# Optimization experiments

Measured on AMD Instinct MI355X. Metric: run time of the kernel, lower is better.

The kernel has to match this reference:

```python
import jax, jax.numpy as jnp
import numpy as np

HID = 2048; NH = 16; NKV = 2; HD = 128; G = NH // NKV
SEC = (16, 24, 24)  # sums to 64 = HD/2
EPS = 1e-6
B, S = 2, 1024


def _reorder(table):
    # table: [3, B, S, HD]; interleave sections picking axis i%3 per chunk
    chunks = []
    idx = 0
    for _ in range(2):
        for sec in SEC:
            chunks.append(table[..., idx:idx + sec])
            idx += sec
    return jnp.concatenate([c[i % len(SEC)] for i, c in enumerate(chunks)], axis=-1)  # [B,S,HD]


def rotate_half(x):
    x1, x2 = jnp.split(x, 2, axis=-1)
    return jnp.concatenate((-x2, x1), axis=-1)


def rms_norm(x, gamma):
    var = jnp.mean(jnp.square(x), axis=-1, keepdims=True)
    return gamma * (x * jax.lax.rsqrt(var + EPS))


def setup_inputs() -> dict:
    key = jax.random.key(0)
    ks = jax.random.split(key, 12)
    x = jax.random.normal(ks[0], (B, S, HID), dtype=jnp.float32)
    ang = jax.random.uniform(ks[1], (3, B, S, HD), dtype=jnp.float32) * 6.28318
    cos = jnp.cos(ang)
    sin = jnp.sin(ang)
    mask = jnp.ones((B, S), dtype=jnp.float32)
    sc = 0.02
    q_w = jax.random.normal(ks[2], (HID, NH * HD), dtype=jnp.float32) * sc
    q_b = jnp.zeros((NH * HD,), dtype=jnp.float32)
    k_w = jax.random.normal(ks[3], (HID, NKV * HD), dtype=jnp.float32) * sc
    k_b = jnp.zeros((NKV * HD,), dtype=jnp.float32)
    v_w = jax.random.normal(ks[4], (HID, NKV * HD), dtype=jnp.float32) * sc
    v_b = jnp.zeros((NKV * HD,), dtype=jnp.float32)
    q_gamma = jnp.ones((HD,), dtype=jnp.float32)
    k_gamma = jnp.ones((HD,), dtype=jnp.float32)
    o_w = jax.random.normal(ks[5], (NH * HD, HID), dtype=jnp.float32) * sc
    return {"x": x, "cos": cos, "sin": sin, "mask": mask,
            "q_w": q_w, "q_b": q_b, "k_w": k_w, "k_b": k_b,
            "v_w": v_w, "v_b": v_b, "q_gamma": q_gamma, "k_gamma": k_gamma,
            "o_w": o_w}


def reference(x, cos, sin, mask, q_w, q_b, k_w, k_b, v_w, v_b, q_gamma, k_gamma, o_w):
    b, s, _ = x.shape
    # QKV projections
    q = (x @ q_w + q_b).reshape(b, s, NH, HD)
    k = (x @ k_w + k_b).reshape(b, s, NKV, HD)
    v = (x @ v_w + v_b).reshape(b, s, NKV, HD)
    # per-head RMSNorm on q, k
    q = rms_norm(q, q_gamma)
    k = rms_norm(k, k_gamma)
    q = jnp.transpose(q, (0, 2, 1, 3))  # [B,NH,S,HD]
    k = jnp.transpose(k, (0, 2, 1, 3))  # [B,NKV,S,HD]
    v = jnp.transpose(v, (0, 2, 1, 3))
    # multimodal RoPE
    cos_f = _reorder(cos)[:, None, :, :]  # [B,1,S,HD]
    sin_f = _reorder(sin)[:, None, :, :]
    q = q * cos_f + rotate_half(q) * sin_f
    k = k * cos_f + rotate_half(k) * sin_f
    # key-mask zeroing and effective lengths
    eff = mask.sum(axis=-1).astype(jnp.int32)  # [B]
    bm = mask[:, None, :, None]
    k = k * bm
    v = v * bm
    hist = (jnp.arange(s)[None, :] < eff[:, None]).astype(jnp.float32)  # [B,S]
    # GQA attention scores in fp32
    qg = q.reshape(b, NKV, G, s, HD)
    scores = jnp.einsum('bngqd,bnkd->bngqk', qg, k,
                        precision=jax.lax.Precision.HIGHEST) * (HD ** -0.5)
    scores = scores.reshape(b, NH, s, s)
    scores = scores + (1.0 - hist)[:, None, None, :] * -1e9
    causal = jnp.tril(jnp.ones((s, s), dtype=jnp.float32))
    scores = scores + (1.0 - causal)[None, None, :, :] * -1e9
    aw = jax.nn.softmax(scores, axis=-1)
    # weighted values
    out = jnp.einsum('bngqk,bnkd->bngqd', aw.reshape(b, NKV, G, s, s), v,
                     precision=jax.lax.Precision.HIGHEST)
    out = out.reshape(b, NH, s, HD)
    out = jnp.transpose(out, (0, 2, 1, 3)).reshape(b, s, NH * HD)
    return out @ o_w
```

## Files before the change

kernel.cpp:

```cpp
#include <hip/hip_runtime.h>

typedef __attribute__((ext_vector_type(8))) short bf16x8;
typedef __attribute__((ext_vector_type(4))) float f32x4;

#define MFMA16(a, b, c) __builtin_amdgcn_mfma_f32_16x16x32_bf16(a, b, c, 0, 0, 0)

__device__ inline short f2bf(float f) {
  union { float f; unsigned u; } v;
  v.f = f;
  unsigned r = v.u + 0x7FFF + ((v.u >> 16) & 1);
  return (short)(r >> 16);
}
__device__ inline float bf2f(short s) {
  union { unsigned u; float f; } v;
  v.u = ((unsigned)(unsigned short)s) << 16;
  return v.f;
}
#define GLD_LDS16(g, l)                                                        \
  __builtin_amdgcn_global_load_lds(                                            \
      (const __attribute__((address_space(1))) unsigned int*)(g),              \
      (__attribute__((address_space(3))) unsigned int*)(l), 16, 0, 0)

__device__ __forceinline__ void raw_barrier() {
  __asm__ volatile("" ::: "memory");
  __builtin_amdgcn_s_barrier();
  __asm__ volatile("" ::: "memory");
}

__global__ __launch_bounds__(256) void prep_kernel(
    const float* __restrict__ x, const float* __restrict__ q_w,
    const float* __restrict__ k_w, const float* __restrict__ v_w,
    const float* __restrict__ o_w, const float* __restrict__ q_b,
    const float* __restrict__ k_b, const float* __restrict__ v_b,
    short* __restrict__ xb, short* __restrict__ wqkv_t, short* __restrict__ wo_t,
    float* __restrict__ biasAll) {
  __shared__ float t[64][65];
  int bid = blockIdx.x;
  if (bid == 6400) {
    for (int i = threadIdx.x; i < 2560; i += 256) {
      float v = (i < 2048) ? q_b[i] : (i < 2304 ? k_b[i - 2048] : v_b[i - 2304]);
      biasAll[i] = v;
    }
    return;
  }
  if (bid < 4096) {
    int i = (bid * 256 + threadIdx.x) * 4;
    float4 f = *(const float4*)&x[i];
    short4 o;
    o.x = f2bf(f.x); o.y = f2bf(f.y); o.z = f2bf(f.z); o.w = f2bf(f.w);
    *(short4*)&xb[i] = o;
    return;
  }
  bid -= 4096;
  const float* src;
  short* dst;
  int C, bx, by;
  if (bid < 1024) {
    src = q_w; dst = wqkv_t; C = 2048;
    bx = (bid & 31) * 64; by = (bid >> 5) * 64;
  } else if (bid < 1152) {
    bid -= 1024;
    src = k_w; dst = wqkv_t + (size_t)2048 * 2048; C = 256;
    bx = (bid & 3) * 64; by = (bid >> 2) * 64;
  } else if (bid < 1280) {
    bid -= 1152;
    src = v_w; dst = wqkv_t + (size_t)2304 * 2048; C = 256;
    bx = (bid & 3) * 64; by = (bid >> 2) * 64;
  } else {
    bid -= 1280;
    src = o_w; dst = wo_t; C = 2048;
    bx = (bid & 31) * 64; by = (bid >> 5) * 64;
  }
  const int R = 2048;
  const int tx = threadIdx.x & 15;
  const int ty = threadIdx.x >> 4;
#pragma unroll
  for (int i = 0; i < 4; i++) {
    int row = ty + i * 16;
    float4 f = *(const float4*)&src[(size_t)(by + row) * C + bx + tx * 4];
    t[row][tx * 4 + 0] = f.x;
    t[row][tx * 4 + 1] = f.y;
    t[row][tx * 4 + 2] = f.z;
    t[row][tx * 4 + 3] = f.w;
  }
  __syncthreads();
#pragma unroll
  for (int i = 0; i < 4; i++) {
    int c = ty + i * 16;
    short4 o;
    o.x = f2bf(t[tx * 4 + 0][c]);
    o.y = f2bf(t[tx * 4 + 1][c]);
    o.z = f2bf(t[tx * 4 + 2][c]);
    o.w = f2bf(t[tx * 4 + 3][c]);
    *(short4*)&dst[(size_t)(bx + c) * R + by + tx * 4] = o;
  }
}

__global__ __launch_bounds__(256) void gemm_qkv_kernel(const short* __restrict__ A,
                                                       const short* __restrict__ B,
                                                       short* __restrict__ Cs,
                                                       const float* __restrict__ bias,
                                                       int N, int gx, int gy, int P) {
  __shared__ __align__(16) short As[4][64 * 32];
  __shared__ __align__(16) short Bs[4][128 * 32];
  const int bid = blockIdx.x;
  const int xcd = bid & 7, idx = bid >> 3;
  const int colsPerX = gx >> 1, rowsPerX = gy >> 2;
  const int xt = (xcd & 1) * colsPerX + idx % colsPerX;
  const int yt = (xcd >> 1) * rowsPerX + idx / colsPerX;
  const int tid = threadIdx.x;
  const int lane = tid & 63, wave = tid >> 6;
  const int quad = lane >> 4, l16 = lane & 15;
  const int m0 = yt * 64, n0 = xt * 128;
  const int wm = (wave >> 1) * 32, wn = (wave & 1) * 64;
  const int r0 = tid >> 2, c0 = (tid & 3) * 8;
  const int ca = ((tid & 3) ^ ((r0 >> 1) & 3)) * 8;
  const size_t arow = (size_t)(m0 + r0) * 2048;
  const size_t brow0 = (size_t)(n0 + r0) * 2048, brow1 = (size_t)(n0 + r0 + 64) * 2048;
  f32x4 acc[2][4];
#pragma unroll
  for (int mi = 0; mi < 2; mi++)
#pragma unroll
    for (int ni = 0; ni < 4; ni++) acc[mi][ni] = (f32x4){0.f, 0.f, 0.f, 0.f};

#pragma unroll
  for (int st = 0; st < 4; st++) {
    const int kk = st * 32 + ca;
    GLD_LDS16(&A[arow + kk], &As[st][r0 * 32 + c0]);
    GLD_LDS16(&B[brow0 + kk], &Bs[st][r0 * 32 + c0]);
    GLD_LDS16(&B[brow1 + kk], &Bs[st][(r0 + 64) * 32 + c0]);
  }

  const int sx = (l16 >> 1) & 3;
  for (int p = 0; p < P; p++) {
    if (p < P - 1) {
      __asm__ volatile("s_waitcnt vmcnt(6)" ::: "memory");
    } else {
      __asm__ volatile("s_waitcnt vmcnt(0)" ::: "memory");
    }
    raw_barrier();
#pragma unroll
    for (int j = 0; j < 2; j++) {
      const int cur = (2 * p + j) & 3;
      bf16x8 af[2], bfr[4];
#pragma unroll
      for (int mi = 0; mi < 2; mi++)
        af[mi] = *(const bf16x8*)&As[cur][(wm + mi * 16 + l16) * 32 + ((quad ^ sx) * 8)];
#pragma unroll
      for (int ni = 0; ni < 4; ni++)
        bfr[ni] = *(const bf16x8*)&Bs[cur][(wn + ni * 16 + l16) * 32 + ((quad ^ sx) * 8)];
#pragma unroll
      for (int mi = 0; mi < 2; mi++)
#pragma unroll
        for (int ni = 0; ni < 4; ni++)
          acc[mi][ni] = MFMA16(af[mi], bfr[ni], acc[mi][ni]);
    }
    __asm__ volatile("s_waitcnt lgkmcnt(0)" ::: "memory");
    raw_barrier();
    if (p < P - 2) {
#pragma unroll
      for (int j = 0; j < 2; j++) {
        const int st = 2 * p + 4 + j;
        const int slot = st & 3;
        const int kk = st * 32 + ca;
        GLD_LDS16(&A[arow + kk], &As[slot][r0 * 32 + c0]);
        GLD_LDS16(&B[brow0 + kk], &Bs[slot][r0 * 32 + c0]);
        GLD_LDS16(&B[brow1 + kk], &Bs[slot][(r0 + 64) * 32 + c0]);
      }
    }
  }
#pragma unroll
  for (int mi = 0; mi < 2; mi++)
#pragma unroll
    for (int ni = 0; ni < 4; ni++) {
      const int col = n0 + wn + ni * 16 + l16;
      const float bv = bias[col];
#pragma unroll
      for (int r = 0; r < 4; r++)
        Cs[(size_t)(m0 + wm + mi * 16 + quad * 4 + r) * N + col] =
            f2bf(acc[mi][ni][r] + bv);
    }
}

__global__ __launch_bounds__(256) void gemm_db_kernel(const short* __restrict__ A,
                                                      const short* __restrict__ B,
                                                      float* __restrict__ C, int N,
                                                      int gx, int gy, int P) {
  __shared__ __align__(16) short As[4][64 * 32];
  __shared__ __align__(16) short Bs[4][128 * 32];
  const int bid = blockIdx.x;
  const int xcd = bid & 7, idx = bid >> 3;
  const int colsPerX = gx >> 1, rowsPerX = gy >> 2;
  const int xt = (xcd & 1) * colsPerX + idx % colsPerX;
  const int yt = (xcd >> 1) * rowsPerX + idx / colsPerX;
  const int tid = threadIdx.x;
  const int lane = tid & 63, wave = tid >> 6;
  const int quad = lane >> 4, l16 = lane & 15;
  const int m0 = yt * 64, n0 = xt * 128;
  const int wm = (wave >> 1) * 32, wn = (wave & 1) * 64;
  const int r0 = tid >> 2, c0 = (tid & 3) * 8;
  const int ca = ((tid & 3) ^ ((r0 >> 1) & 3)) * 8;
  const size_t arow = (size_t)(m0 + r0) * 2048;
  const size_t brow0 = (size_t)(n0 + r0) * 2048, brow1 = (size_t)(n0 + r0 + 64) * 2048;
  f32x4 acc[2][4];
#pragma unroll
  for (int mi = 0; mi < 2; mi++)
#pragma unroll
    for (int ni = 0; ni < 4; ni++) acc[mi][ni] = (f32x4){0.f, 0.f, 0.f, 0.f};

#pragma unroll
  for (int st = 0; st < 4; st++) {
    const int kk = st * 32 + ca;
    GLD_LDS16(&A[arow + kk], &As[st][r0 * 32 + c0]);
    GLD_LDS16(&B[brow0 + kk], &Bs[st][r0 * 32 + c0]);
    GLD_LDS16(&B[brow1 + kk], &Bs[st][(r0 + 64) * 32 + c0]);
  }

  const int sx = (l16 >> 1) & 3;
  for (int p = 0; p < P; p++) {
    if (p < P - 1) {
      __asm__ volatile("s_waitcnt vmcnt(6)" ::: "memory");
    } else {
      __asm__ volatile("s_waitcnt vmcnt(0)" ::: "memory");
    }
    raw_barrier();
#pragma unroll
    for (int j = 0; j < 2; j++) {
      const int cur = (2 * p + j) & 3;
      bf16x8 af[2], bfr[4];
#pragma unroll
      for (int mi = 0; mi < 2; mi++)
        af[mi] = *(const bf16x8*)&As[cur][(wm + mi * 16 + l16) * 32 + ((quad ^ sx) * 8)];
#pragma unroll
      for (int ni = 0; ni < 4; ni++)
        bfr[ni] = *(const bf16x8*)&Bs[cur][(wn + ni * 16 + l16) * 32 + ((quad ^ sx) * 8)];
#pragma unroll
      for (int mi = 0; mi < 2; mi++)
#pragma unroll
        for (int ni = 0; ni < 4; ni++)
          acc[mi][ni] = MFMA16(af[mi], bfr[ni], acc[mi][ni]);
    }
    __asm__ volatile("s_waitcnt lgkmcnt(0)" ::: "memory");
    raw_barrier();
    if (p < P - 2) {
#pragma unroll
      for (int j = 0; j < 2; j++) {
        const int st = 2 * p + 4 + j;
        const int slot = st & 3;
        const int kk = st * 32 + ca;
        GLD_LDS16(&A[arow + kk], &As[slot][r0 * 32 + c0]);
        GLD_LDS16(&B[brow0 + kk], &Bs[slot][r0 * 32 + c0]);
        GLD_LDS16(&B[brow1 + kk], &Bs[slot][(r0 + 64) * 32 + c0]);
      }
    }
  }
#pragma unroll
  for (int mi = 0; mi < 2; mi++)
#pragma unroll
    for (int ni = 0; ni < 4; ni++)
#pragma unroll
      for (int r = 0; r < 4; r++)
        C[(size_t)(m0 + wm + mi * 16 + quad * 4 + r) * N + n0 + wn + ni * 16 + l16] =
            acc[mi][ni][r];
}

__global__ __launch_bounds__(256) void postv_kv_kernel(
    const short* __restrict__ qkvb, const float* __restrict__ kg,
    const float* __restrict__ cosb, const float* __restrict__ sinb,
    const float* __restrict__ maskp, short* __restrict__ ko, short* __restrict__ vtb) {
  __shared__ short t[32][33];
  const int bid = blockIdx.x;
  if (bid < 1024) {
    const int rid = bid * 4 + (threadIdx.x >> 6);
    const int lane = threadIdx.x & 63;
    const int slot = rid >> 11;
    const int bs = rid & 2047;
    const int b = bs >> 10, s = bs & 1023;
    const short* row = qkvb + (size_t)bs * 2560 + 2048 + slot * 128;
    float v0 = bf2f(row[lane]);
    float v1 = bf2f(row[64 + lane]);
    float ss = v0 * v0 + v1 * v1;
#pragma unroll
    for (int o = 1; o < 64; o <<= 1) ss += __shfl_xor(ss, o);
    float r = rsqrtf(ss * (1.0f / 128.0f) + 1e-6f);
    v0 = kg[lane] * v0 * r;
    v1 = kg[64 + lane] * v1 * r;
    int sel = (lane < 16) ? 0 : (lane < 40) ? 1 : 2;
    size_t ci = ((size_t)(sel * 2 + b) * 1024 + s) * 128 + lane;
    float c0 = cosb[ci], s0 = sinb[ci], c1 = cosb[ci + 64], s1 = sinb[ci + 64];
    const float mk = maskp[bs];
    float o0 = (v0 * c0 - v1 * s0) * mk;
    float o1 = (v1 * c1 + v0 * s1) * mk;
    short* dst = ko + (((size_t)(b * 2 + slot) * 1024) + s) * 128;
    dst[lane] = f2bf(o0);
    dst[64 + lane] = f2bf(o1);
    return;
  }
  const int b2 = bid - 1024;
  const int d0 = (b2 & 3) * 32;
  const int s0 = ((b2 >> 2) & 31) * 32;
  const int bz = b2 >> 7;
  const int bq = bz >> 1, kv = bz & 1;
  const int tx = threadIdx.x & 31;
  const int ty = threadIdx.x >> 5;
#pragma unroll
  for (int i = 0; i < 4; i++) {
    int s = s0 + ty + i * 8;
    size_t qi = ((size_t)(bq * 1024 + s)) * 2560 + 2304 + kv * 128 + d0 + tx;
    float val = bf2f(qkvb[qi]);
    t[ty + i * 8][tx] = f2bf(val * maskp[bq * 1024 + s]);
  }
  __syncthreads();
#pragma unroll
  for (int i = 0; i < 4; i++)
    vtb[((size_t)bz * 128 + d0 + ty + i * 8) * 1024 + s0 + tx] = t[tx][ty + i * 8];
}

__global__ __launch_bounds__(256) void attn_kernel(
    const short* __restrict__ qkvb, const short* __restrict__ K,
    const short* __restrict__ Vt_g, const float* __restrict__ qg,
    const float* __restrict__ cosb, const float* __restrict__ sinb,
    short* __restrict__ attn) {
  const int qt = 15 - (int)blockIdx.x;
  const int h = blockIdx.y;
  const int b = blockIdx.z;
  const int nsteps = qt + 1;

  const int kv = h >> 3;
  const int tid = threadIdx.x;
  const int wave = tid >> 6, lane = tid & 63;
  const int quad = lane >> 4, l16 = lane & 15;
  __shared__ __align__(16) short Ks[2][64 * 128];
  __shared__ __align__(16) short Vs[2][128 * 64];
  __shared__ __align__(16) short Ps[4][16 * 72];

  const size_t koff = ((size_t)(b * 2 + kv) * 1024) * 128;
  const size_t voff = koff;
  const float scale = 0.08838834764831845f;

#define STAGE_KV(bf, ks0)                                                          \
  {                                                                                \
    _Pragma("unroll") for (int it = 0; it < 4; it++) {                             \
      const int c = it * 256 + tid;                                                \
      const int row = c >> 4, sl = c & 15;                                         \
      GLD_LDS16(&K[koff + (size_t)((ks0) + row) * 128 + ((sl ^ (row & 7)) * 8)],   \
                &Ks[bf][c * 8]);                                                   \
      const int d = c >> 3, sv = c & 7;                                            \
      GLD_LDS16(&Vt_g[voff + (size_t)d * 1024 + (ks0) + ((sv ^ (d & 7)) * 8)],     \
                &Vs[bf][c * 8]);                                                   \
    }                                                                              \
  }

  STAGE_KV(0, 0);

  const int s = qt * 64 + wave * 16 + l16;
  const short* qrow = qkvb + ((size_t)(b * 1024 + s)) * 2560 + h * 128;
  bf16x8 qraw[4];
#pragma unroll
  for (int kk = 0; kk < 4; kk++) qraw[kk] = *(const bf16x8*)&qrow[kk * 32 + quad * 8];
  float vq[4][8];
  float ss = 0.f;
#pragma unroll
  for (int kk = 0; kk < 4; kk++)
#pragma unroll
    for (int e = 0; e < 8; e++) {
      vq[kk][e] = bf2f(qraw[kk][e]);
      ss = fmaf(vq[kk][e], vq[kk][e], ss);
    }
  ss += __shfl_xor(ss, 16);
  ss += __shfl_xor(ss, 32);
  const float rr = rsqrtf(ss * (1.0f / 128.0f) + 1e-6f);
#pragma unroll
  for (int kk = 0; kk < 4; kk++) {
    float4 ga = *(const float4*)&qg[kk * 32 + quad * 8];
    float4 gb = *(const float4*)&qg[kk * 32 + quad * 8 + 4];
    vq[kk][0] *= ga.x * rr; vq[kk][1] *= ga.y * rr;
    vq[kk][2] *= ga.z * rr; vq[kk][3] *= ga.w * rr;
    vq[kk][4] *= gb.x * rr; vq[kk][5] *= gb.y * rr;
    vq[kk][6] *= gb.z * rr; vq[kk][7] *= gb.w * rr;
  }
  bf16x8 aq[4];
#pragma unroll
  for (int kk = 0; kk < 2; kk++) {
    const int dbase = kk * 32 + quad * 8;
    const int sel = (dbase < 16) ? 0 : (dbase < 40) ? 1 : 2;
    const size_t ci = ((size_t)(sel * 2 + b) * 1024 + s) * 128 + dbase;
    float cd[8], sd[8], cD[8], sD[8];
    {
      float4 a0 = *(const float4*)&cosb[ci], a1 = *(const float4*)&cosb[ci + 4];
      cd[0]=a0.x; cd[1]=a0.y; cd[2]=a0.z; cd[3]=a0.w;
      cd[4]=a1.x; cd[5]=a1.y; cd[6]=a1.z; cd[7]=a1.w;
    }
    {
      float4 a0 = *(const float4*)&sinb[ci], a1 = *(const float4*)&sinb[ci + 4];
      sd[0]=a0.x; sd[1]=a0.y; sd[2]=a0.z; sd[3]=a0.w;
      sd[4]=a1.x; sd[5]=a1.y; sd[6]=a1.z; sd[7]=a1.w;
    }
    {
      float4 a0 = *(const float4*)&cosb[ci + 64], a1 = *(const float4*)&cosb[ci + 68];
      cD[0]=a0.x; cD[1]=a0.y; cD[2]=a0.z; cD[3]=a0.w;
      cD[4]=a1.x; cD[5]=a1.y; cD[6]=a1.z; cD[7]=a1.w;
    }
    {
      float4 a0 = *(const float4*)&sinb[ci + 64], a1 = *(const float4*)&sinb[ci + 68];
      sD[0]=a0.x; sD[1]=a0.y; sD[2]=a0.z; sD[3]=a0.w;
      sD[4]=a1.x; sD[5]=a1.y; sD[6]=a1.z; sD[7]=a1.w;
    }
#pragma unroll
    for (int e = 0; e < 8; e++) {
      aq[kk][e] = f2bf(vq[kk][e] * cd[e] - vq[kk + 2][e] * sd[e]);
      aq[kk + 2][e] = f2bf(vq[kk + 2][e] * cD[e] + vq[kk][e] * sD[e]);
    }
  }

  f32x4 o[8];
#pragma unroll
  for (int i = 0; i < 8; i++) o[i] = (f32x4){0.f, 0.f, 0.f, 0.f};
  float l[4] = {0.f, 0.f, 0.f, 0.f};
  const int qrow0 = qt * 64 + wave * 16 + quad * 4;

  for (int st = 0; st < nsteps; st++) {
    __asm__ volatile("s_waitcnt vmcnt(0)" ::: "memory");
    raw_barrier();
    if (st + 1 < nsteps) { STAGE_KV((st + 1) & 1, (st + 1) * 64); }
    const int cb = st & 1;
    const int ks0 = st * 64;
    f32x4 sc[4];
#pragma unroll
    for (int nt = 0; nt < 4; nt++) sc[nt] = (f32x4){0.f, 0.f, 0.f, 0.f};
    __builtin_amdgcn_s_setprio(1);
#pragma unroll
    for (int nt = 0; nt < 4; nt++) {
      const int rrK = nt * 16 + l16;
#pragma unroll
      for (int kk = 0; kk < 4; kk++) {
        bf16x8 bk = *(const bf16x8*)&Ks[cb][rrK * 128 + (((kk * 4 + quad) ^ (rrK & 7)) * 8)];
        sc[nt] = MFMA16(aq[kk], bk, sc[nt]);
      }
    }
    __builtin_amdgcn_s_setprio(0);
    short* P = &Ps[wave][0];
#pragma unroll
    for (int nt = 0; nt < 4; nt++) {
      const int kcol = ks0 + nt * 16 + l16;
#pragma unroll
      for (int r = 0; r < 4; r++) {
        float p = (kcol > qrow0 + r) ? 0.f : __expf(fmaf(sc[nt][r], scale, -12.0f));
        l[r] += p;
        P[(quad * 4 + r) * 72 + nt * 16 + l16] = f2bf(p);
      }
    }
    __asm__ volatile("s_waitcnt lgkmcnt(0)" ::: "memory");
    bf16x8 pa0 = *(const bf16x8*)&P[l16 * 72 + quad * 8];
    bf16x8 pa1 = *(const bf16x8*)&P[l16 * 72 + 32 + quad * 8];
    __builtin_amdgcn_s_setprio(1);
#pragma unroll
    for (int nt = 0; nt < 8; nt++) {
      const int rrV = nt * 16 + l16;
      bf16x8 bv0 = *(const bf16x8*)&Vs[cb][rrV * 64 + ((quad ^ (rrV & 7)) * 8)];
      bf16x8 bv1 = *(const bf16x8*)&Vs[cb][rrV * 64 + (((4 + quad) ^ (rrV & 7)) * 8)];
      o[nt] = MFMA16(pa0, bv0, o[nt]);
      o[nt] = MFMA16(pa1, bv1, o[nt]);
    }
    __builtin_amdgcn_s_setprio(0);
  }
#undef STAGE_KV
#pragma unroll
  for (int off = 1; off < 16; off <<= 1)
#pragma unroll
    for (int r = 0; r < 4; r++) l[r] += __shfl_xor(l[r], off);
  float inv[4];
#pragma unroll
  for (int r = 0; r < 4; r++) inv[r] = 1.f / l[r];
  const int lrow = wave * 16 + quad * 4;
  short* dst = attn + ((size_t)(b * 1024 + qt * 64 + lrow)) * 2048 + h * 128;
#pragma unroll
  for (int nt = 0; nt < 8; nt++)
#pragma unroll
    for (int r = 0; r < 4; r++)
      dst[(size_t)r * 2048 + nt * 16 + l16] = f2bf(o[nt][r] * inv[r]);
}

extern "C" void kernel_launch(void* const* d_in, const int* in_sizes, int n_in,
                              void* d_out, int out_size, void* d_ws, size_t ws_size,
                              hipStream_t stream) {
  const float* x = (const float*)d_in[0];
  const float* cosb = (const float*)d_in[1];
  const float* sinb = (const float*)d_in[2];
  const float* mask = (const float*)d_in[3];
  const float* q_w = (const float*)d_in[4];
  const float* q_b = (const float*)d_in[5];
  const float* k_w = (const float*)d_in[6];
  const float* k_b = (const float*)d_in[7];
  const float* v_w = (const float*)d_in[8];
  const float* v_b = (const float*)d_in[9];
  const float* qg = (const float*)d_in[10];
  const float* kg = (const float*)d_in[11];
  const float* o_w = (const float*)d_in[12];
  float* out = (float*)d_out;

  char* ws = (char*)d_ws;
  short* wo_t = (short*)(ws);
  short* wqkv_t = (short*)(ws + ((size_t)8 << 20));
  short* attn = (short*)(ws + ((size_t)9 << 20));
  short* xb = (short*)(ws + ((size_t)18 << 20));
  short* kb = (short*)(ws + ((size_t)46 << 20));
  short* vtb = (short*)(ws + ((size_t)47 << 20));
  short* qkvb = (short*)(ws + ((size_t)48 << 20));
  float* biasAll = (float*)(ws + ((size_t)68 << 20));

  prep_kernel<<<6401, 256, 0, stream>>>(x, q_w, k_w, v_w, o_w, q_b, k_b, v_b, xb,
                                        wqkv_t, wo_t, biasAll);
  gemm_qkv_kernel<<<640, 256, 0, stream>>>(xb, wqkv_t, qkvb, biasAll, 2560, 20, 32, 32);
  postv_kv_kernel<<<1536, 256, 0, stream>>>(qkvb, kg, cosb, sinb, mask, kb, vtb);
  attn_kernel<<<dim3(16, 16, 2), 256, 0, stream>>>(qkvb, kb, vtb, qg, cosb, sinb, attn);
  gemm_db_kernel<<<512, 256, 0, stream>>>(attn, wo_t, out, 2048, 16, 32, 32);
}
```

Measured before the change: 221.2 us.

## Fuse K norm/RoPE/mask and V transpose into QKV GEMM epilogue

Removes the separate postv_kv kernel and does the K per-head RMSNorm, RoPE and masking, plus the masked V transpose, in the QKV GEMM epilogue for column tiles 16-19. The tile is staged through the reused LDS buffer. This saves one launch and a round trip of the K/V columns through global memory. In exchange, those epilogue blocks run longer and serial per-wave loops, which may imbalance the GEMM tail.

```diff
diff --git a/kernel.cpp b/kernel.cpp
--- a/kernel.cpp
+++ b/kernel.cpp
@@ -96,13 +96,15 @@
   }
 }
 
-__global__ __launch_bounds__(256) void gemm_qkv_kernel(const short* __restrict__ A,
-                                                       const short* __restrict__ B,
-                                                       short* __restrict__ Cs,
-                                                       const float* __restrict__ bias,
-                                                       int N, int gx, int gy, int P) {
-  __shared__ __align__(16) short As[4][64 * 32];
-  __shared__ __align__(16) short Bs[4][128 * 32];
+__global__ __launch_bounds__(256) void gemm_qkv_kernel(
+    const short* __restrict__ A, const short* __restrict__ B,
+    short* __restrict__ Cs, const float* __restrict__ bias,
+    const float* __restrict__ kg, const float* __restrict__ cosb,
+    const float* __restrict__ sinb, const float* __restrict__ maskp,
+    short* __restrict__ ko, short* __restrict__ vtb, int gx, int gy, int P) {
+  __shared__ __align__(16) short sm[4 * 64 * 32 + 4 * 128 * 32];
+#define AsP(st) (&sm[(st)*2048])
+#define BsP(st) (&sm[8192 + (st)*4096])
   const int bid = blockIdx.x;
   const int xcd = bid & 7, idx = bid >> 3;
   const int colsPerX = gx >> 1, rowsPerX = gy >> 2;
@@ -126,9 +128,9 @@
 #pragma unroll
   for (int st = 0; st < 4; st++) {
     const int kk = st * 32 + ca;
-    GLD_LDS16(&A[arow + kk], &As[st][r0 * 32 + c0]);
-    GLD_LDS16(&B[brow0 + kk], &Bs[st][r0 * 32 + c0]);
-    GLD_LDS16(&B[brow1 + kk], &Bs[st][(r0 + 64) * 32 + c0]);
+    GLD_LDS16(&A[arow + kk], AsP(st) + r0 * 32 + c0);
+    GLD_LDS16(&B[brow0 + kk], BsP(st) + r0 * 32 + c0);
+    GLD_LDS16(&B[brow1 + kk], BsP(st) + (r0 + 64) * 32 + c0);
   }
 
   const int sx = (l16 >> 1) & 3;
@@ -145,10 +147,10 @@
       bf16x8 af[2], bfr[4];
 #pragma unroll
       for (int mi = 0; mi < 2; mi++)
-        af[mi] = *(const bf16x8*)&As[cur][(wm + mi * 16 + l16) * 32 + ((quad ^ sx) * 8)];
+        af[mi] = *(const bf16x8*)(AsP(cur) + (wm + mi * 16 + l16) * 32 + ((quad ^ sx) * 8));
 #pragma unroll
       for (int ni = 0; ni < 4; ni++)
-        bfr[ni] = *(const bf16x8*)&Bs[cur][(wn + ni * 16 + l16) * 32 + ((quad ^ sx) * 8)];
+        bfr[ni] = *(const bf16x8*)(BsP(cur) + (wn + ni * 16 + l16) * 32 + ((quad ^ sx) * 8));
 #pragma unroll
       for (int mi = 0; mi < 2; mi++)
 #pragma unroll
@@ -163,23 +165,91 @@
         const int st = 2 * p + 4 + j;
         const int slot = st & 3;
         const int kk = st * 32 + ca;
-        GLD_LDS16(&A[arow + kk], &As[slot][r0 * 32 + c0]);
-        GLD_LDS16(&B[brow0 + kk], &Bs[slot][r0 * 32 + c0]);
-        GLD_LDS16(&B[brow1 + kk], &Bs[slot][(r0 + 64) * 32 + c0]);
+        GLD_LDS16(&A[arow + kk], AsP(slot) + r0 * 32 + c0);
+        GLD_LDS16(&B[brow0 + kk], BsP(slot) + r0 * 32 + c0);
+        GLD_LDS16(&B[brow1 + kk], BsP(slot) + (r0 + 64) * 32 + c0);
       }
     }
   }
+
+  if (xt < 16) {
+#pragma unroll
+    for (int mi = 0; mi < 2; mi++)
+#pragma unroll
+      for (int ni = 0; ni < 4; ni++) {
+        const int col = n0 + wn + ni * 16 + l16;
+        const float bv = bias[col];
+#pragma unroll
+        for (int r = 0; r < 4; r++)
+          Cs[(size_t)(m0 + wm + mi * 16 + quad * 4 + r) * 2560 + col] =
+              f2bf(acc[mi][ni][r] + bv);
+      }
+    return;
+  }
+
+  const int bb = m0 >> 10, sg = m0 & 1023;
+  short* Ts = sm;
 #pragma unroll
   for (int mi = 0; mi < 2; mi++)
 #pragma unroll
     for (int ni = 0; ni < 4; ni++) {
-      const int col = n0 + wn + ni * 16 + l16;
-      const float bv = bias[col];
+      const int col = wn + ni * 16 + l16;
+      const float bv = bias[n0 + col];
 #pragma unroll
       for (int r = 0; r < 4; r++)
-        Cs[(size_t)(m0 + wm + mi * 16 + quad * 4 + r) * N + col] =
-            f2bf(acc[mi][ni][r] + bv);
-    }
+        Ts[(wm + mi * 16 + quad * 4 + r) * 136 + col] = f2bf(acc[mi][ni][r] + bv);
+    }
+  __syncthreads();
+
+  if (xt < 18) {
+    const int slot = xt - 16;
+    const float g0 = kg[lane], g1 = kg[64 + lane];
+    const int sel = (lane < 16) ? 0 : (lane < 40) ? 1 : 2;
+    const size_t cbase = ((size_t)(sel * 2 + bb) * 1024 + sg + wave * 16) * 128 + lane;
+    float c0n = cosb[cbase], s0n = sinb[cbase];
+    float c1n = cosb[cbase + 64], s1n = sinb[cbase + 64];
+    float mkn = maskp[m0 + wave * 16];
+#pragma unroll
+    for (int i = 0; i < 16; i++) {
+      const float c0v = c0n, s0v = s0n, c1v = c1n, s1v = s1n, mk = mkn;
+      if (i < 15) {
+        const size_t cn = cbase + (size_t)(i + 1) * 128;
+        c0n = cosb[cn]; s0n = sinb[cn];
+        c1n = cosb[cn + 64]; s1n = sinb[cn + 64];
+        mkn = maskp[m0 + wave * 16 + i + 1];
+      }
+      const int row = wave * 16 + i;
+      const int s = sg + row;
+      float v0 = bf2f(Ts[row * 136 + lane]);
+      float v1 = bf2f(Ts[row * 136 + 64 + lane]);
+      float ssum = v0 * v0 + v1 * v1;
+#pragma unroll
+      for (int o = 1; o < 64; o <<= 1) ssum += __shfl_xor(ssum, o);
+      const float rr = rsqrtf(ssum * (1.0f / 128.0f) + 1e-6f);
+      v0 = g0 * v0 * rr;
+      v1 = g1 * v1 * rr;
+      const float o0 = (v0 * c0v - v1 * s0v) * mk;
+      const float o1 = (v1 * c1v + v0 * s1v) * mk;
+      short* dst = ko + (((size_t)(bb * 2 + slot) * 1024) + s) * 128;
+      dst[lane] = f2bf(o0);
+      dst[64 + lane] = f2bf(o1);
+    }
+  } else {
+    const int kvs = xt - 18;
+    const int d = tid >> 1;
+    const int sb = (tid & 1) * 32;
+    short tmp[32];
+#pragma unroll
+    for (int i = 0; i < 32; i++) {
+      const int srow = sb + i;
+      tmp[i] = f2bf(bf2f(Ts[srow * 136 + d]) * maskp[m0 + srow]);
+    }
+    short* dst = vtb + ((size_t)(bb * 2 + kvs) * 128 + d) * 1024 + sg + sb;
+#pragma unroll
+    for (int j = 0; j < 4; j++) *(int4*)&dst[j * 8] = *(const int4*)&tmp[j * 8];
+  }
+#undef AsP
+#undef BsP
 }
 
 __global__ __launch_bounds__(256) void gemm_db_kernel(const short* __restrict__ A,
@@ -264,58 +334,6 @@
             acc[mi][ni][r];
 }
 
-__global__ __launch_bounds__(256) void postv_kv_kernel(
-    const short* __restrict__ qkvb, const float* __restrict__ kg,
-    const float* __restrict__ cosb, const float* __restrict__ sinb,
-    const float* __restrict__ maskp, short* __restrict__ ko, short* __restrict__ vtb) {
-  __shared__ short t[32][33];
-  const int bid = blockIdx.x;
-  if (bid < 1024) {
-    const int rid = bid * 4 + (threadIdx.x >> 6);
-    const int lane = threadIdx.x & 63;
-    const int slot = rid >> 11;
-    const int bs = rid & 2047;
-    const int b = bs >> 10, s = bs & 1023;
-    const short* row = qkvb + (size_t)bs * 2560 + 2048 + slot * 128;
-    float v0 = bf2f(row[lane]);
-    float v1 = bf2f(row[64 + lane]);
-    float ss = v0 * v0 + v1 * v1;
-#pragma unroll
-    for (int o = 1; o < 64; o <<= 1) ss += __shfl_xor(ss, o);
-    float r = rsqrtf(ss * (1.0f / 128.0f) + 1e-6f);
-    v0 = kg[lane] * v0 * r;
-    v1 = kg[64 + lane] * v1 * r;
-    int sel = (lane < 16) ? 0 : (lane < 40) ? 1 : 2;
-    size_t ci = ((size_t)(sel * 2 + b) * 1024 + s) * 128 + lane;
-    float c0 = cosb[ci], s0 = sinb[ci], c1 = cosb[ci + 64], s1 = sinb[ci + 64];
-    const float mk = maskp[bs];
-    float o0 = (v0 * c0 - v1 * s0) * mk;
-    float o1 = (v1 * c1 + v0 * s1) * mk;
-    short* dst = ko + (((size_t)(b * 2 + slot) * 1024) + s) * 128;
-    dst[lane] = f2bf(o0);
-    dst[64 + lane] = f2bf(o1);
-    return;
-  }
-  const int b2 = bid - 1024;
-  const int d0 = (b2 & 3) * 32;
-  const int s0 = ((b2 >> 2) & 31) * 32;
-  const int bz = b2 >> 7;
-  const int bq = bz >> 1, kv = bz & 1;
-  const int tx = threadIdx.x & 31;
-  const int ty = threadIdx.x >> 5;
-#pragma unroll
-  for (int i = 0; i < 4; i++) {
-    int s = s0 + ty + i * 8;
-    size_t qi = ((size_t)(bq * 1024 + s)) * 2560 + 2304 + kv * 128 + d0 + tx;
-    float val = bf2f(qkvb[qi]);
-    t[ty + i * 8][tx] = f2bf(val * maskp[bq * 1024 + s]);
-  }
-  __syncthreads();
-#pragma unroll
-  for (int i = 0; i < 4; i++)
-    vtb[((size_t)bz * 128 + d0 + ty + i * 8) * 1024 + s0 + tx] = t[tx][ty + i * 8];
-}
-
 __global__ __launch_bounds__(256) void attn_kernel(
     const short* __restrict__ qkvb, const short* __restrict__ K,
     const short* __restrict__ Vt_g, const float* __restrict__ qg,
@@ -511,8 +529,8 @@
 
   prep_kernel<<<6401, 256, 0, stream>>>(x, q_w, k_w, v_w, o_w, q_b, k_b, v_b, xb,
                                         wqkv_t, wo_t, biasAll);
-  gemm_qkv_kernel<<<640, 256, 0, stream>>>(xb, wqkv_t, qkvb, biasAll, 2560, 20, 32, 32);
-  postv_kv_kernel<<<1536, 256, 0, stream>>>(qkvb, kg, cosb, sinb, mask, kb, vtb);
+  gemm_qkv_kernel<<<640, 256, 0, stream>>>(xb, wqkv_t, qkvb, biasAll, kg, cosb, sinb,
+                                           mask, kb, vtb, 20, 32, 32);
   attn_kernel<<<dim3(16, 16, 2), 256, 0, stream>>>(qkvb, kb, vtb, qg, cosb, sinb, attn);
   gemm_db_kernel<<<512, 256, 0, stream>>>(attn, wo_t, out, 2048, 16, 32, 32);
 }
```

After: 226.0 us. +2.2%, slower.
